# Optimization experiments

Hardware: AMD Instinct MI355X
Metric: run time of the kernel (lower is better)

## Reference

```python
import jax, jax.numpy as jnp
import numpy as np

H = 1024      # hidden_dim
NH = 8        # num_heads
DH = H // NH  # head dim = 128
IN = 512      # in_state_dim
CD = 256      # cond_dim
OUT = 512     # out_motion_dim
FH = 128      # FiLM hidden (hard-coded in _CondFiLM)
CLIP = 16.0   # input_clip
B, T = 2048, 32


def _ln(x, g, b, eps=1e-5):
    m = jnp.mean(x, axis=-1, keepdims=True)
    v = jnp.var(x, axis=-1, keepdims=True)
    return (x - m) * jax.lax.rsqrt(v + eps) * g + b


def setup_inputs() -> dict:
    key = jax.random.key(0)
    ks = jax.random.split(key, 16)
    w = lambda k, s: jax.random.normal(k, s, dtype=jnp.float32) * 0.02
    D = IN + CD
    return {
        'state': jax.random.normal(ks[0], (B, T, IN), dtype=jnp.float32),
        'cond': jax.random.normal(ks[1], (B, T, CD), dtype=jnp.float32),
        # shared_encoder: [Linear -> LayerNorm -> ReLU] x 2
        'ew1': w(ks[2], (D, H)), 'eb1': jnp.zeros((H,)), 'eg1': jnp.ones((H,)), 'ebt1': jnp.zeros((H,)),
        'ew2': w(ks[3], (H, H)), 'eb2': jnp.zeros((H,)), 'eg2': jnp.ones((H,)), 'ebt2': jnp.zeros((H,)),
        # residual_proj (input_dim != hidden_dim -> Linear)
        'rw': w(ks[4], (D, H)), 'rb': jnp.zeros((H,)),
        # FiLM conditioner
        'fw1': w(ks[5], (CD, FH)), 'fb1': jnp.zeros((FH,)),
        'fw2': w(ks[6], (FH, 2 * H)), 'fb2': jnp.zeros((2 * H,)),
        # query LayerNorm
        'lnq_g': jnp.ones((H,)), 'lnq_b': jnp.zeros((H,)),
        # attention projections (bias=False)
        'wq': w(ks[7], (H, H)), 'wk': w(ks[8], (H, H)), 'wv': w(ks[9], (H, H)), 'wo': w(ks[10], (H, H)),
        # coupling norm
        'cn_g': jnp.ones((H,)), 'cn_b': jnp.zeros((H,)),
        # motion head: Linear -> ReLU -> Linear
        'hw1': w(ks[11], (H, H)), 'hb1': jnp.zeros((H,)),
        'hw2': w(ks[12], (H, OUT)), 'hb2': jnp.zeros((OUT,)),
    }


def reference(state, cond, ew1, eb1, eg1, ebt1, ew2, eb2, eg2, ebt2, rw, rb,
              fw1, fb1, fw2, fb2, lnq_g, lnq_b, wq, wk, wv, wo, cn_g, cn_b,
              hw1, hb1, hw2, hb2):
    # input concat + guard clamp
    x = jnp.clip(jnp.concatenate([state, cond], axis=-1), -CLIP, CLIP)  # [B,T,D]
    # shared encoder
    h = jax.nn.relu(_ln(x @ ew1 + eb1, eg1, ebt1))
    h = jax.nn.relu(_ln(h @ ew2 + eb2, eg2, ebt2))                       # [B,T,H]
    res = x @ rw + rb                                                    # [B,T,H]
    # FiLM gain/bias from cond (exact-erf gelu to match torch F.gelu)
    fh = jax.nn.gelu(cond @ fw1 + fb1, approximate=False)
    g, b = jnp.split(fh @ fw2 + fb2, 2, axis=-1)
    g = 1.0 + 0.5 * jnp.tanh(g)
    b = 0.5 * jnp.tanh(b)
    # FiLM-gated query path
    qin = _ln(h, lnq_g, lnq_b) * g + b
    Bq, Tq, _ = h.shape
    q = (qin @ wq).reshape(Bq, Tq, NH, DH)
    k = (h @ wk).reshape(Bq, Tq, NH, DH)
    v = (h @ wv).reshape(Bq, Tq, NH, DH)
    scores = jnp.einsum('bqhd,bkhd->bhqk', q, k) / np.float32(np.sqrt(DH))
    attn = jax.nn.softmax(scores, axis=-1)
    o = jnp.einsum('bhqk,bkhd->bqhd', attn, v).reshape(Bq, Tq, H) @ wo
    # residual couple + norm
    h2 = _ln(h + o + res, cn_g, cn_b)
    # motion head
    m = jax.nn.relu(h2 @ hw1 + hb1)
    return m @ hw2 + hb2  # [B,T,out_motion_dim]
```

## Files before the change

### kernel.cpp

```cpp
#include <hip/hip_runtime.h>
#include <hip/hip_bf16.h>

typedef unsigned short u16;
typedef short bf16x8 __attribute__((ext_vector_type(8)));
typedef u16 u16x8 __attribute__((ext_vector_type(8)));
typedef float f32x4 __attribute__((ext_vector_type(4)));
typedef float f32x16 __attribute__((ext_vector_type(16)));

#define DEV __device__ __forceinline__

DEV u16 f2bf(float f) {
  union { float f; unsigned u; } a; a.f = f;
  unsigned r = a.u + 0x7FFFu + ((a.u >> 16) & 1u);
  return (u16)(r >> 16);
}
DEV float bf2f(u16 u) {
  union { unsigned u; float f; } a; a.u = ((unsigned)u) << 16; return a.f;
}
DEV float ftanh(float v) {
  float e = __expf(2.f * v);
  return 1.f - 2.f / (e + 1.f);
}
DEV void async16(const void* g, void* l) {
  __builtin_amdgcn_global_load_lds(
      (const __attribute__((address_space(1))) unsigned int*)g,
      (__attribute__((address_space(3))) unsigned int*)l, 16, 0, 0);
}

#define SBAR() asm volatile("s_barrier" ::: "memory")
#define WAITV(n) asm volatile("s_waitcnt vmcnt(" #n ")" ::: "memory")

__global__ __launch_bounds__(256) void transpose_cvt(const float* __restrict__ in,
                                                     u16* __restrict__ out, int K, int N) {
  __shared__ float tile[32][33];
  const int kt = blockIdx.y * 32, nt = blockIdx.x * 32;
  const int tx = threadIdx.x & 31, ty = threadIdx.x >> 5;
#pragma unroll
  for (int i = 0; i < 32; i += 8) {
    int k = kt + ty + i, n = nt + tx;
    tile[ty + i][tx] = (k < K && n < N) ? in[(long)k * N + n] : 0.f;
  }
  __syncthreads();
#pragma unroll
  for (int i = 0; i < 32; i += 8) {
    int n = nt + ty + i, k = kt + tx;
    if (n < N && k < K) out[(long)n * K + k] = f2bf(tile[tx][ty + i]);
  }
}

__global__ __launch_bounds__(256) void prep_kernel(const float* __restrict__ state,
                                                   const float* __restrict__ cond,
                                                   u16* __restrict__ xb) {
  int idx = blockIdx.x * 256 + threadIdx.x;
  int t = idx / 192, c4 = idx - t * 192;
  float4 v;
  if (c4 < 128) v = ((const float4*)state)[(long)t * 128 + c4];
  else          v = ((const float4*)cond)[(long)t * 64 + (c4 - 128)];
  ushort4 o;
  o.x = f2bf(fminf(fmaxf(v.x, -16.f), 16.f));
  o.y = f2bf(fminf(fmaxf(v.y, -16.f), 16.f));
  o.z = f2bf(fminf(fmaxf(v.z, -16.f), 16.f));
  o.w = f2bf(fminf(fmaxf(v.w, -16.f), 16.f));
  *(ushort4*)(xb + (long)t * 768 + c4 * 4) = o;
}

struct WSrc { const float* p[11]; };
__global__ __launch_bounds__(256) void init_kernel(WSrc src, u16* __restrict__ wt,
                                                   const float* __restrict__ state,
                                                   const float* __restrict__ cond,
                                                   u16* __restrict__ xb) {
  __shared__ float tile[32][33];
  const int b = blockIdx.x;
  if (b >= 8480) {
    int idx = (b - 8480) * 256 + threadIdx.x;
    int t = idx / 192, c4 = idx - t * 192;
    float4 v;
    if (c4 < 128) v = ((const float4*)state)[(long)t * 128 + c4];
    else          v = ((const float4*)cond)[(long)t * 64 + (c4 - 128)];
    ushort4 o;
    o.x = f2bf(fminf(fmaxf(v.x, -16.f), 16.f));
    o.y = f2bf(fminf(fmaxf(v.y, -16.f), 16.f));
    o.z = f2bf(fminf(fmaxf(v.z, -16.f), 16.f));
    o.w = f2bf(fminf(fmaxf(v.w, -16.f), 16.f));
    *(ushort4*)(xb + (long)t * 768 + c4 * 4) = o;
    return;
  }
  int job, base, K, N, X;
  long off;
  if      (b < 768)  { job = 0;  base = 0;    K = 768;  N = 1024; X = 32; off = 0; }
  else if (b < 1536) { job = 1;  base = 768;  K = 768;  N = 1024; X = 32; off = 786432; }
  else if (b < 2560) { job = 2;  base = 1536; K = 1024; N = 1024; X = 32; off = 1572864; }
  else if (b < 2592) { job = 3;  base = 2560; K = 256;  N = 128;  X = 4;  off = 2621440; }
  else if (b < 2848) { job = 4;  base = 2592; K = 128;  N = 2048; X = 64; off = 2654208; }
  else if (b < 3872) { job = 5;  base = 2848; K = 1024; N = 1024; X = 32; off = 2916352; }
  else if (b < 4896) { job = 6;  base = 3872; K = 1024; N = 1024; X = 32; off = 3964928; }
  else if (b < 5920) { job = 7;  base = 4896; K = 1024; N = 1024; X = 32; off = 5013504; }
  else if (b < 6944) { job = 8;  base = 5920; K = 1024; N = 1024; X = 32; off = 6062080; }
  else if (b < 7968) { job = 9;  base = 6944; K = 1024; N = 1024; X = 32; off = 7110656; }
  else               { job = 10; base = 7968; K = 1024; N = 512;  X = 16; off = 8159232; }
  const float* in = src.p[job];
  u16* out = wt + off;
  const int lb = b - base;
  const int kt = (lb / X) * 32, nt = (lb % X) * 32;
  const int tx = threadIdx.x & 31, ty = threadIdx.x >> 5;
#pragma unroll
  for (int i = 0; i < 32; i += 8) {
    int k = kt + ty + i, n = nt + tx;
    tile[ty + i][tx] = (k < K && n < N) ? in[(long)k * N + n] : 0.f;
  }
  __syncthreads();
#pragma unroll
  for (int i = 0; i < 32; i += 8) {
    int n = nt + ty + i, k = kt + tx;
    if (n < N && k < K) out[(long)n * K + k] = f2bf(tile[tx][ty + i]);
  }
}

DEV void wreduce2(float& s, float& q) {
#pragma unroll
  for (int off = 32; off; off >>= 1) { s += __shfl_xor(s, off); q += __shfl_xor(q, off); }
}

__global__ __launch_bounds__(256) void ln_relu_w(const u16* in,
                                                 const float* __restrict__ g,
                                                 const float* __restrict__ bt,
                                                 u16* out) {
  const int wid = threadIdx.x >> 6, lane = threadIdx.x & 63;
  const long row = (long)blockIdx.x * 4 + wid;
  const u16* ip = in + row * 1024 + lane * 16;
  u16x8 v0 = *(const u16x8*)ip;
  u16x8 v1 = *(const u16x8*)(ip + 8);
  float x[16];
#pragma unroll
  for (int j = 0; j < 8; ++j) { x[j] = bf2f(v0[j]); x[8 + j] = bf2f(v1[j]); }
  float s = 0.f, q = 0.f;
#pragma unroll
  for (int j = 0; j < 16; ++j) { s += x[j]; q += x[j] * x[j]; }
  wreduce2(s, q);
  float mean = s * (1.f / 1024.f);
  float var  = q * (1.f / 1024.f) - mean * mean;
  float rs   = rsqrtf(var + 1e-5f);
  const int c0 = lane * 16;
  float4 g0 = *(const float4*)(g + c0),      g1 = *(const float4*)(g + c0 + 4);
  float4 g2 = *(const float4*)(g + c0 + 8),  g3 = *(const float4*)(g + c0 + 12);
  float4 b0 = *(const float4*)(bt + c0),     b1 = *(const float4*)(bt + c0 + 4);
  float4 b2 = *(const float4*)(bt + c0 + 8), b3 = *(const float4*)(bt + c0 + 12);
  float ga[16] = {g0.x,g0.y,g0.z,g0.w, g1.x,g1.y,g1.z,g1.w, g2.x,g2.y,g2.z,g2.w, g3.x,g3.y,g3.z,g3.w};
  float ba[16] = {b0.x,b0.y,b0.z,b0.w, b1.x,b1.y,b1.z,b1.w, b2.x,b2.y,b2.z,b2.w, b3.x,b3.y,b3.z,b3.w};
  u16x8 o0, o1;
#pragma unroll
  for (int j = 0; j < 8; ++j) {
    o0[j] = f2bf(fmaxf((x[j] - mean) * rs * ga[j] + ba[j], 0.f));
    o1[j] = f2bf(fmaxf((x[8 + j] - mean) * rs * ga[8 + j] + ba[8 + j], 0.f));
  }
  u16* op = out + row * 1024 + lane * 16;
  *(u16x8*)op = o0;
  *(u16x8*)(op + 8) = o1;
}

__global__ __launch_bounds__(256) void h2_w(const u16* __restrict__ h,
                                            const u16* o2,
                                            const float* __restrict__ g,
                                            const float* __restrict__ bt,
                                            u16* out) {
  const int wid = threadIdx.x >> 6, lane = threadIdx.x & 63;
  const long row = (long)blockIdx.x * 4 + wid;
  const u16* hp = h + row * 1024 + lane * 16;
  const u16* op2 = o2 + row * 1024 + lane * 16;
  u16x8 a0 = *(const u16x8*)hp,  a1 = *(const u16x8*)(hp + 8);
  u16x8 c0v = *(const u16x8*)op2, c1v = *(const u16x8*)(op2 + 8);
  float x[16];
#pragma unroll
  for (int j = 0; j < 8; ++j) {
    x[j]     = bf2f(a0[j]) + bf2f(c0v[j]);
    x[8 + j] = bf2f(a1[j]) + bf2f(c1v[j]);
  }
  float s = 0.f, q = 0.f;
#pragma unroll
  for (int j = 0; j < 16; ++j) { s += x[j]; q += x[j] * x[j]; }
  wreduce2(s, q);
  float mean = s * (1.f / 1024.f);
  float var  = q * (1.f / 1024.f) - mean * mean;
  float rs   = rsqrtf(var + 1e-5f);
  const int cc = lane * 16;
  u16x8 o0, o1;
#pragma unroll
  for (int j = 0; j < 8; ++j) {
    o0[j] = f2bf((x[j] - mean) * rs * g[cc + j] + bt[cc + j]);
    o1[j] = f2bf((x[8 + j] - mean) * rs * g[cc + 8 + j] + bt[cc + 8 + j]);
  }
  u16* op = out + row * 1024 + lane * 16;
  *(u16x8*)op = o0;
  *(u16x8*)(op + 8) = o1;
}

__global__ __launch_bounds__(256) void qin_sep_kernel(const u16* __restrict__ h,
                                                      const u16* gain, const u16* bias,
                                                      const float* __restrict__ lg,
                                                      const float* __restrict__ lbt,
                                                      u16* qout) {
  __shared__ float sh[8];
  const long row = blockIdx.x;
  const int tid = threadIdx.x;
  ushort4 hv = *(const ushort4*)(h + row * 1024 + tid * 4);
  float x[4] = {bf2f(hv.x), bf2f(hv.y), bf2f(hv.z), bf2f(hv.w)};
  float s = x[0] + x[1] + x[2] + x[3];
  float q = x[0]*x[0] + x[1]*x[1] + x[2]*x[2] + x[3]*x[3];
#pragma unroll
  for (int off = 32; off; off >>= 1) { s += __shfl_xor(s, off); q += __shfl_xor(q, off); }
  const int w = tid >> 6;
  if ((tid & 63) == 0) { sh[w] = s; sh[4 + w] = q; }
  __syncthreads();
  s = sh[0] + sh[1] + sh[2] + sh[3];
  q = sh[4] + sh[5] + sh[6] + sh[7];
  float mean = s * (1.f / 1024.f);
  float var  = q * (1.f / 1024.f) - mean * mean;
  float rs   = rsqrtf(var + 1e-5f);
  ushort4 gv = *(const ushort4*)(gain + row * 1024 + tid * 4);
  ushort4 bv = *(const ushort4*)(bias + row * 1024 + tid * 4);
  const u16* gp = (const u16*)&gv;
  const u16* bp = (const u16*)&bv;
  ushort4 ov; u16* op = (u16*)&ov;
#pragma unroll
  for (int j = 0; j < 4; ++j) {
    int c = tid * 4 + j;
    float y = (x[j] - mean) * rs * lg[c] + lbt[c];
    op[j] = f2bf(y * bf2f(gp[j]) + bf2f(bp[j]));
  }
  *(ushort4*)(qout + row * 1024 + tid * 4) = ov;
}

__global__ __launch_bounds__(256) void film_qin(const u16* __restrict__ hbf,
                                                const u16* __restrict__ fh,
                                                const u16* __restrict__ fw2T,
                                                const float* __restrict__ fb2,
                                                const float* __restrict__ lg,
                                                const float* __restrict__ lbt,
                                                u16* __restrict__ qout) {
  extern __shared__ char lds[];
  u16* H = (u16*)lds;
  char* Afh = lds + 65536;
  float* sLN = (float*)(lds + 73728);
  const int tid = threadIdx.x;
  const int wid = tid >> 6, lane = tid & 63;
  const int fr = lane & 15, fq = lane >> 4;
  const long rows0 = (long)blockIdx.x * 32;

  {
    const int row = tid >> 3;
    const int inner = (tid & 7) * 32;
    const u16* src = fh + (rows0 + row) * 128 + (tid & 7) * 16;
    u16x8 f0 = *(const u16x8*)src;
    u16x8 f1 = *(const u16x8*)(src + 8);
    *(u16x8*)(Afh + row * 256 + ((inner)      ^ ((row & 7) << 4))) = f0;
    *(u16x8*)(Afh + row * 256 + ((inner + 16) ^ ((row & 7) << 4))) = f1;
  }

#pragma unroll
  for (int i = 0; i < 8; ++i) {
    const int row = i * 4 + wid;
    const u16* src = hbf + (rows0 + row) * 1024 + lane * 16;
    u16x8 v0 = *(const u16x8*)src;
    u16x8 v1 = *(const u16x8*)(src + 8);
    *(u16x8*)(H + row * 1024 + lane * 16) = v0;
    *(u16x8*)(H + row * 1024 + lane * 16 + 8) = v1;
    float s = 0.f, q = 0.f;
#pragma unroll
    for (int j = 0; j < 8; ++j) {
      float x0 = bf2f(v0[j]), x1 = bf2f(v1[j]);
      s += x0 + x1; q += x0 * x0 + x1 * x1;
    }
    wreduce2(s, q);
    if (lane == 0) {
      float mean = s * (1.f / 1024.f);
      float var  = q * (1.f / 1024.f) - mean * mean;
      sLN[row * 2] = mean;
      sLN[row * 2 + 1] = rsqrtf(var + 1e-5f);
    }
  }
  __syncthreads();

  const int cbase = wid * 256;
#pragma unroll 1
  for (int c8 = 0; c8 < 16; ++c8) {
    const int c = cbase + c8 * 16;
    const int col = c + fr;
    f32x4 ag[2] = {{0.f,0.f,0.f,0.f},{0.f,0.f,0.f,0.f}};
    f32x4 ab[2] = {{0.f,0.f,0.f,0.f},{0.f,0.f,0.f,0.f}};
#pragma unroll
    for (int ks = 0; ks < 4; ++ks) {
      bf16x8 bg = *(const bf16x8*)(fw2T + (long)col * 128 + ks * 32 + fq * 8);
      bf16x8 bb = *(const bf16x8*)(fw2T + (long)(1024 + col) * 128 + ks * 32 + fq * 8);
#pragma unroll
      for (int t = 0; t < 2; ++t) {
        const int row = t * 16 + fr;
        bf16x8 av = *(const bf16x8*)(Afh + row * 256 + ((ks * 64 + fq * 16) ^ ((fr & 7) << 4)));
        ag[t] = __builtin_amdgcn_mfma_f32_16x16x32_bf16(av, bg, ag[t], 0, 0, 0);
        ab[t] = __builtin_amdgcn_mfma_f32_16x16x32_bf16(av, bb, ab[t], 0, 0, 0);
      }
    }
    const float fg = fb2[col], fb = fb2[1024 + col];
    const float lgc = lg[col], lbc = lbt[col];
#pragma unroll
    for (int t = 0; t < 2; ++t)
#pragma unroll
      for (int r = 0; r < 4; ++r) {
        const int row = t * 16 + fq * 4 + r;
        float gv = 1.f + 0.5f * ftanh(ag[t][r] + fg);
        float bv = 0.5f * ftanh(ab[t][r] + fb);
        float x = bf2f(H[row * 1024 + col]);
        float y = (x - sLN[row * 2]) * sLN[row * 2 + 1] * lgc + lbc;
        H[row * 1024 + col] = f2bf(y * gv + bv);
      }
  }
  __syncthreads();

#pragma unroll
  for (int i = 0; i < 8; ++i) {
    const int row = i * 4 + wid;
    u16* dst = qout + (rows0 + row) * 1024 + lane * 16;
    *(u16x8*)dst = *(const u16x8*)(H + row * 1024 + lane * 16);
    *(u16x8*)(dst + 8) = *(const u16x8*)(H + row * 1024 + lane * 16 + 8);
  }
}

template <int EPI>
__global__ __launch_bounds__(256) void gemm_bt(const u16* __restrict__ A,
                                               const u16* __restrict__ Bt,
                                               const float* __restrict__ bias,
                                               const u16* addend,
                                               u16* Co, float* Cf,
                                               int N, int K, int lda) {
  __shared__ u16 As[128 * 64];
  __shared__ u16 Bs[128 * 64];
  const int tid = threadIdx.x;
  const int w = tid >> 6, l = tid & 63;
  const int wr = w >> 1, wc = w & 1;
  const long bRow = (long)blockIdx.x * 128;
  const long bCol = (long)blockIdx.y * 128;

  f32x4 acc[4][4];
#pragma unroll
  for (int mi = 0; mi < 4; ++mi)
#pragma unroll
    for (int ni = 0; ni < 4; ++ni) acc[mi][ni] = (f32x4){0.f, 0.f, 0.f, 0.f};

  const int arow = l >> 3;
  const int acol = (l & 7) * 8;
  const u16* gA = A + (bRow + w * 8 + arow) * (long)lda + acol;
  const u16* gB = Bt + (bCol + w * 8 + arow) * (long)K + acol;

  const int fr = l & 15;
  const int fks = (l >> 4) * 8;

  for (int kt = 0; kt < K; kt += 64) {
#pragma unroll
    for (int i = 0; i < 4; ++i) {
      async16(gA + (long)i * 32 * lda + kt, As + (i * 32 + w * 8) * 64);
      async16(gB + (long)i * 32 * K   + kt, Bs + (i * 32 + w * 8) * 64);
    }
    __syncthreads();
#pragma unroll
    for (int kk = 0; kk < 2; ++kk) {
      const int ko = kk * 32 + fks;
      bf16x8 af[4], bff[4];
#pragma unroll
      for (int mi = 0; mi < 4; ++mi)
        af[mi] = *(const bf16x8*)(As + (wr * 64 + mi * 16 + fr) * 64 + ko);
#pragma unroll
      for (int ni = 0; ni < 4; ++ni)
        bff[ni] = *(const bf16x8*)(Bs + (wc * 64 + ni * 16 + fr) * 64 + ko);
#pragma unroll
      for (int mi = 0; mi < 4; ++mi)
#pragma unroll
        for (int ni = 0; ni < 4; ++ni)
          acc[mi][ni] = __builtin_amdgcn_mfma_f32_16x16x32_bf16(af[mi], bff[ni], acc[mi][ni], 0, 0, 0);
    }
    __syncthreads();
  }

  const int fq = l >> 4;
#pragma unroll
  for (int ni = 0; ni < 4; ++ni) {
    const long col = bCol + wc * 64 + ni * 16 + fr;
    const float bs = bias ? bias[col] : 0.f;
#pragma unroll
    for (int mi = 0; mi < 4; ++mi) {
#pragma unroll
      for (int r = 0; r < 4; ++r) {
        const long row = bRow + wr * 64 + mi * 16 + fq * 4 + r;
        float v = acc[mi][ni][r] + bs;
        if (EPI == 1) v = 0.5f * v * (1.f + erff(v * 0.70710678118654752f));
        else if (EPI == 2) v = 1.f + 0.5f * ftanh(v);
        else if (EPI == 3) v = fmaxf(v, 0.f);
        else if (EPI == 5) v += bf2f(addend[row * N + col]);
        else if (EPI == 6) v = 0.5f * ftanh(v);
        if (EPI == 4) Cf[row * N + col] = v;
        else          Co[row * N + col] = f2bf(v);
      }
    }
  }
}


#define RDA(buf, Qr) do { \
  _Pragma("unroll") for (int ks_ = 0; ks_ < 2; ++ks_) \
  _Pragma("unroll") for (int m_ = 0; m_ < 4; ++m_) \
    a[ks_][m_] = *(const bf16x8*)(ldsc + (buf) * 32768 + \
      ((Qr) * 128 + wr * 64 + m_ * 16 + fr) * 128 + ((ks_ * 64 + fq * 16) ^ swzc)); \
} while (0)

#define RDB(buf, Qc, bb) do { \
  _Pragma("unroll") for (int ks_ = 0; ks_ < 2; ++ks_) \
  _Pragma("unroll") for (int n_ = 0; n_ < 2; ++n_) \
    bb[ks_][n_] = *(const bf16x8*)(ldsc + 65536 + (buf) * 32768 + \
      ((Qc) * 128 + wc * 32 + n_ * 16 + fr) * 128 + ((ks_ * 64 + fq * 16) ^ swzc)); \
} while (0)

#define MM(Qr, Qc, bb) do { \
  __builtin_amdgcn_s_setprio(1); \
  _Pragma("unroll") for (int m_ = 0; m_ < 4; ++m_) \
  _Pragma("unroll") for (int n_ = 0; n_ < 2; ++n_) \
  _Pragma("unroll") for (int ks_ = 0; ks_ < 2; ++ks_) \
    acc[Qr][Qc][m_][n_] = __builtin_amdgcn_mfma_f32_16x16x32_bf16( \
        a[ks_][m_], bb[ks_][n_], acc[Qr][Qc][m_][n_], 0, 0, 0); \
  __builtin_amdgcn_s_setprio(0); \
} while (0)

#define STA(buf, tt, h) do { \
  _Pragma("unroll") for (int j_ = 0; j_ < 2; ++j_) \
    async16(aB + ((long)j_ * 64 + (h) * 128) * lda_l + (tt) * 64, \
            ldsc + (buf) * 32768 + (h) * 16384 + (j_ * 512 + tid) * 16); \
} while (0)

#define STB(buf, tt, h) do { \
  _Pragma("unroll") for (int j_ = 0; j_ < 2; ++j_) \
    async16(bB + ((long)j_ * 64 + (h) * 128) * K_l + (tt) * 64, \
            ldsc + 65536 + (buf) * 32768 + (h) * 16384 + (j_ * 512 + tid) * 16); \
} while (0)

template <int EPI>
__global__ __launch_bounds__(512, 2) void gemm256(const u16* __restrict__ A,
                                                  const u16* __restrict__ Bt,
                                                  const float* __restrict__ bias,
                                                  const u16* addend,
                                                  u16* Co, u16* Co2, float* Cf,
                                                  int N, int K, int lda, int ctLog) {
  extern __shared__ char ldsc[];
  const int tid = threadIdx.x;
  const int l = tid & 63;
  const int w = tid >> 6, wr = w >> 2, wc = w & 3;
  const int fr = l & 15, fq = l >> 4;
  const int swzc = (fr & 7) << 4;
  const long lda_l = lda, K_l = K;

  const int nwg = gridDim.x;
  const int orig = blockIdx.x;
  const int swz = (orig & 7) * (nwg >> 3) + (orig >> 3);
  const int rt = swz >> ctLog, ct = swz & ((1 << ctLog) - 1);
  const long bRow = (long)rt * 256, bCol = (long)ct * 256;
  const int NT = K >> 6;

  const int L0 = tid * 16;
  const int row0 = L0 >> 7;
  const int cswz = (L0 & 127) ^ ((row0 & 7) << 4);
  const u16* aB = A + (bRow + row0) * lda_l + (cswz >> 1);
  const u16* bB = Bt + (bCol + row0) * K_l + (cswz >> 1);

  f32x4 acc[2][2][4][2];
#pragma unroll
  for (int p = 0; p < 2; ++p)
#pragma unroll
    for (int qq = 0; qq < 2; ++qq)
#pragma unroll
      for (int m = 0; m < 4; ++m)
#pragma unroll
        for (int n = 0; n < 2; ++n) acc[p][qq][m][n] = (f32x4){0.f, 0.f, 0.f, 0.f};

  bf16x8 a[2][4], b0[2][2], b1[2][2];

  STA(0, 0, 0); STA(0, 0, 1); STB(0, 0, 0); STB(0, 0, 1);
  STA(1, 1, 0); STB(1, 1, 1);
  WAITV(4);
  SBAR();

  for (int i = 0; i < (NT >> 1); ++i) {
    const int t0 = 2 * i, t1 = t0 + 1;
    const bool more = (t0 + 2) < NT;
    RDA(0, 0); RDB(0, 0, b0); RDB(0, 1, b1);
    STA(1, t1, 1); STB(1, t1, 0);
    SBAR(); MM(0, 0, b0); MM(0, 1, b1); SBAR();
    RDA(0, 1);
    if (more) { STA(0, t0 + 2, 0); STB(0, t0 + 2, 1); }
    SBAR(); MM(1, 1, b1); MM(1, 0, b0);
    if (more) { WAITV(4); } else { WAITV(0); }
    SBAR();
    RDA(1, 0); RDB(1, 0, b0); RDB(1, 1, b1);
    if (more) { STA(0, t0 + 2, 1); STB(0, t0 + 2, 0); }
    SBAR(); MM(0, 0, b0); MM(0, 1, b1); SBAR();
    RDA(1, 1);
    if (more) { STA(1, t1 + 2, 0); STB(1, t1 + 2, 1); }
    SBAR(); MM(1, 1, b1); MM(1, 0, b0);
    if (more) { WAITV(4); } else { WAITV(0); }
    SBAR();
  }

  if (EPI != 4) {
    u16* dst = Co; long colBase = bCol; long strideW = N;
    if (EPI == 6) {
      strideW = 1024;
      if (bCol >= 1024) { dst = Co2; colBase = bCol - 1024; }
    }
    u16* lds16 = (u16*)ldsc;
#pragma unroll
    for (int Qr = 0; Qr < 2; ++Qr)
#pragma unroll
      for (int Qc = 0; Qc < 2; ++Qc)
#pragma unroll
        for (int n = 0; n < 2; ++n) {
          const int colL = Qc * 128 + wc * 32 + n * 16 + fr;
          const float bs = bias ? bias[bCol + colL] : 0.f;
#pragma unroll
          for (int m = 0; m < 4; ++m)
#pragma unroll
            for (int r = 0; r < 4; ++r) {
              const int rowL = Qr * 128 + wr * 64 + m * 16 + fq * 4 + r;
              float v = acc[Qr][Qc][m][n][r] + bs;
              if (EPI == 3) v = fmaxf(v, 0.f);
              lds16[rowL * 256 + colL] = f2bf(v);
            }
        }
    __syncthreads();
    const int rB = tid >> 5, cL = (tid & 31) * 8;
#pragma unroll
    for (int it = 0; it < 16; ++it) {
      const int rL = it * 16 + rB;
      const long gr = bRow + rL;
      u16x8 sv = *(const u16x8*)(lds16 + rL * 256 + cL);
      if (EPI == 5) {
        u16x8 ad = *(const u16x8*)(addend + gr * (long)N + bCol + cL);
#pragma unroll
        for (int j = 0; j < 8; ++j) sv[j] = f2bf(bf2f(sv[j]) + bf2f(ad[j]));
      }
      *(u16x8*)(dst + gr * strideW + colBase + cL) = sv;
    }
  } else {
    float* ldsf = (float*)ldsc;
#pragma unroll
    for (int p = 0; p < 2; ++p) {
#pragma unroll
      for (int Qc = 0; Qc < 2; ++Qc)
#pragma unroll
        for (int n = 0; n < 2; ++n) {
          const int colL = Qc * 128 + wc * 32 + n * 16 + fr;
          const float bs = bias ? bias[bCol + colL] : 0.f;
#pragma unroll
          for (int m = 0; m < 4; ++m)
#pragma unroll
            for (int r = 0; r < 4; ++r) {
              const int rowL = wr * 64 + m * 16 + fq * 4 + r;
              ldsf[rowL * 256 + colL] = acc[p][Qc][m][n][r] + bs;
            }
        }
      __syncthreads();
      const int c4 = (tid & 63) * 4, rB = tid >> 6;
#pragma unroll
      for (int it = 0; it < 16; ++it) {
        const int rL = it * 8 + rB;
        const long gr = bRow + p * 128 + rL;
        float4 fv = *(const float4*)(ldsf + rL * 256 + c4);
        *(float4*)(Cf + gr * (long)N + bCol + c4) = fv;
      }
      __syncthreads();
    }
  }
}

__global__ __launch_bounds__(256) void attn4_kernel(const u16* q,
                                                    const u16* __restrict__ k,
                                                    const u16* __restrict__ v,
                                                    u16* o) {
  const int tid = threadIdx.x;
  const int wid = tid >> 6, l = tid & 63;
  const int bh = blockIdx.x * 4 + wid;
  const int b = bh >> 3, hd = bh & 7;
  const long base = (long)b * 32 * 1024 + hd * 128;
  const int lo = l & 31, hi = l >> 5;
  __shared__ u16 P[4][32 * 36];
  __shared__ u16 Vt[4][128 * 36];
  u16* Pw = P[wid];
  u16* Vw = Vt[wid];

#pragma unroll
  for (int i = 0; i < 8; ++i) {
    int idx = i * 64 + l;
    int tok = idx >> 4, d0 = (idx & 15) * 8;
    const u16* src = v + base + (long)tok * 1024 + d0;
    ushort4 a0 = *(const ushort4*)src;
    ushort4 a1 = *(const ushort4*)(src + 4);
    u16 vals[8] = {a0.x, a0.y, a0.z, a0.w, a1.x, a1.y, a1.z, a1.w};
#pragma unroll
    for (int j = 0; j < 8; ++j) Vw[(d0 + j) * 36 + tok] = vals[j];
  }

  f32x16 st;
#pragma unroll
  for (int r = 0; r < 16; ++r) st[r] = 0.f;
#pragma unroll
  for (int kb = 0; kb < 8; ++kb) {
    bf16x8 kf = *(const bf16x8*)(k + base + (long)lo * 1024 + kb * 16 + hi * 8);
    bf16x8 qf = *(const bf16x8*)(q + base + (long)lo * 1024 + kb * 16 + hi * 8);
    st = __builtin_amdgcn_mfma_f32_32x32x16_bf16(kf, qf, st, 0, 0, 0);
  }
  float mx = -1e30f;
#pragma unroll
  for (int r = 0; r < 16; ++r) { st[r] *= 0.08838834764831845f; mx = fmaxf(mx, st[r]); }
  mx = fmaxf(mx, __shfl_xor(mx, 32));
  float p[16], sum = 0.f;
#pragma unroll
  for (int r = 0; r < 16; ++r) { p[r] = __expf(st[r] - mx); sum += p[r]; }
  sum += __shfl_xor(sum, 32);
  const float inv = 1.f / sum;
#pragma unroll
  for (int r = 0; r < 16; ++r) {
    int kt = (r & 3) + 8 * (r >> 2) + 4 * hi;
    Pw[lo * 36 + kt] = f2bf(p[r] * inv);
  }
  __syncthreads();

#pragma unroll
  for (int nb = 0; nb < 4; ++nb) {
    f32x16 oa;
#pragma unroll
    for (int r = 0; r < 16; ++r) oa[r] = 0.f;
#pragma unroll
    for (int ks = 0; ks < 2; ++ks) {
      union { bf16x8 v8; ushort4 h[2]; } pa, vb;
      pa.h[0] = *(const ushort4*)&Pw[lo * 36 + ks * 16 + hi * 8];
      pa.h[1] = *(const ushort4*)&Pw[lo * 36 + ks * 16 + hi * 8 + 4];
      vb.h[0] = *(const ushort4*)&Vw[(nb * 32 + lo) * 36 + ks * 16 + hi * 8];
      vb.h[1] = *(const ushort4*)&Vw[(nb * 32 + lo) * 36 + ks * 16 + hi * 8 + 4];
      oa = __builtin_amdgcn_mfma_f32_32x32x16_bf16(pa.v8, vb.v8, oa, 0, 0, 0);
    }
#pragma unroll
    for (int r = 0; r < 16; ++r) {
      int qrow = (r & 3) + 8 * (r >> 2) + 4 * hi;
      o[base + (long)qrow * 1024 + nb * 32 + lo] = f2bf(oa[r]);
    }
  }
}

extern "C" void kernel_launch(void* const* d_in, const int* in_sizes, int n_in,
                              void* d_out, int out_size, void* d_ws, size_t ws_size,
                              hipStream_t stream) {
  const float* state = (const float*)d_in[0];  const float* cond  = (const float*)d_in[1];
  const float* ew1 = (const float*)d_in[2];    const float* eb1 = (const float*)d_in[3];
  const float* eg1 = (const float*)d_in[4];    const float* ebt1 = (const float*)d_in[5];
  const float* ew2 = (const float*)d_in[6];    const float* eb2 = (const float*)d_in[7];
  const float* eg2 = (const float*)d_in[8];    const float* ebt2 = (const float*)d_in[9];
  const float* rw = (const float*)d_in[10];    const float* rb = (const float*)d_in[11];
  const float* fw1 = (const float*)d_in[12];   const float* fb1 = (const float*)d_in[13];
  const float* fw2 = (const float*)d_in[14];   const float* fb2 = (const float*)d_in[15];
  const float* lnq_g = (const float*)d_in[16]; const float* lnq_b = (const float*)d_in[17];
  const float* wq = (const float*)d_in[18];    const float* wk = (const float*)d_in[19];
  const float* wv = (const float*)d_in[20];    const float* wo = (const float*)d_in[21];
  const float* cn_g = (const float*)d_in[22];  const float* cn_b = (const float*)d_in[23];
  const float* hw1 = (const float*)d_in[24];   const float* hb1 = (const float*)d_in[25];
  const float* hw2 = (const float*)d_in[26];   const float* hb2 = (const float*)d_in[27];

  const size_t MB128 = 134217728ULL;
  const size_t WT_BYTES = 17367040ULL;
  const size_t FH_BYTES = 16777216ULL;
  char* ws = (char*)d_ws;
  u16* OUTu = (u16*)d_out;
  float* OUTf = (float*)d_out;

  (void)hipFuncSetAttribute((const void*)gemm256<0>, hipFuncAttributeMaxDynamicSharedMemorySize, 131072);
  (void)hipFuncSetAttribute((const void*)gemm256<3>, hipFuncAttributeMaxDynamicSharedMemorySize, 131072);
  (void)hipFuncSetAttribute((const void*)gemm256<4>, hipFuncAttributeMaxDynamicSharedMemorySize, 131072);
  (void)hipFuncSetAttribute((const void*)gemm256<5>, hipFuncAttributeMaxDynamicSharedMemorySize, 131072);
  (void)hipFuncSetAttribute((const void*)gemm256<6>, hipFuncAttributeMaxDynamicSharedMemorySize, 131072);
  (void)hipFuncSetAttribute((const void*)film_qin,   hipFuncAttributeMaxDynamicSharedMemorySize, 73984);

  u16* wt = nullptr;
  bool planA = false;
  int R = 0;
  if (ws_size >= 3 * MB128 + FH_BYTES + WT_BYTES) {
    planA = true;
    wt = (u16*)(ws + 3 * MB128 + FH_BYTES);
  } else {
    for (int r = 8192; r >= 1024; r >>= 1) {
      size_t need = 2 * MB128 + (size_t)r * 8448ULL + WT_BYTES;
      if (ws_size >= need) { R = r; wt = (u16*)(ws + 2 * MB128 + (size_t)r * 8448ULL); break; }
    }
    if (!R) return;
  }

  u16* ew1T = wt + 0;        u16* rwT  = wt + 786432;  u16* ew2T = wt + 1572864;
  u16* fw1T = wt + 2621440;  u16* fw2T = wt + 2654208;
  u16* wqT  = wt + 2916352;  u16* wkT  = wt + 3964928; u16* wvT  = wt + 5013504;
  u16* woT  = wt + 6062080;  u16* hw1T = wt + 7110656; u16* hw2T = wt + 8159232;

  if (planA) {
    u16* S1 = (u16*)ws;
    u16* S2 = (u16*)(ws + MB128);
    u16* S3 = (u16*)(ws + 2 * MB128);
    u16* FH = (u16*)(ws + 3 * MB128);

    WSrc src;
    src.p[0] = ew1; src.p[1] = rw;  src.p[2] = ew2; src.p[3] = fw1; src.p[4] = fw2;
    src.p[5] = wq;  src.p[6] = wk;  src.p[7] = wv;  src.p[8] = wo;  src.p[9] = hw1;
    src.p[10] = hw2;
    init_kernel<<<57632, 256, 0, stream>>>(src, wt, state, cond, S1);

    gemm_bt<1><<<dim3(512, 1), 256, 0, stream>>>(S1 + 512, fw1T, fb1, nullptr, FH, nullptr, 128, 256, 768);
    gemm256<0><<<1024, 512, 131072, stream>>>(S1, ew1T, eb1, nullptr, S2, nullptr, nullptr, 1024, 768, 768, 2);
    ln_relu_w<<<16384, 256, 0, stream>>>(S2, eg1, ebt1, S2);
    gemm256<0><<<1024, 512, 131072, stream>>>(S2, ew2T, eb2, nullptr, S3, nullptr, nullptr, 1024, 1024, 1024, 2);
    ln_relu_w<<<16384, 256, 0, stream>>>(S3, eg2, ebt2, S3);
    film_qin<<<2048, 256, 73984, stream>>>(S3, FH, fw2T, fb2, lnq_g, lnq_b, OUTu);
    gemm256<0><<<1024, 512, 131072, stream>>>(OUTu, wqT, nullptr, nullptr, S1, nullptr, nullptr, 1024, 1024, 1024, 2);
    gemm256<6><<<2048, 512, 131072, stream>>>(S3, wkT, nullptr, nullptr, S2, OUTu, nullptr, 2048, 1024, 1024, 3);
    attn4_kernel<<<4096, 256, 0, stream>>>(S1, S2, OUTu, S1);
    prep_kernel<<<49152, 256, 0, stream>>>(state, cond, S2);
    gemm256<0><<<1024, 512, 131072, stream>>>(S2, rwT, rb, nullptr, OUTu, nullptr, nullptr, 1024, 768, 768, 2);
    gemm256<5><<<1024, 512, 131072, stream>>>(S1, woT, nullptr, OUTu, OUTu, nullptr, nullptr, 1024, 1024, 1024, 2);
    h2_w<<<16384, 256, 0, stream>>>(S3, OUTu, cn_g, cn_b, S1);
    gemm256<3><<<1024, 512, 131072, stream>>>(S1, hw1T, hb1, nullptr, S2, nullptr, nullptr, 1024, 1024, 1024, 2);
    gemm256<4><<<512, 512, 131072, stream>>>(S2, hw2T, hb2, nullptr, nullptr, nullptr, OUTf, 512, 1024, 1024, 1);
    return;
  }

  transpose_cvt<<<dim3(32, 24), 256, 0, stream>>>(ew1, ew1T, 768, 1024);
  transpose_cvt<<<dim3(32, 24), 256, 0, stream>>>(rw,  rwT,  768, 1024);
  transpose_cvt<<<dim3(32, 32), 256, 0, stream>>>(ew2, ew2T, 1024, 1024);
  transpose_cvt<<<dim3(4, 8),   256, 0, stream>>>(fw1, fw1T, 256, 128);
  transpose_cvt<<<dim3(64, 4),  256, 0, stream>>>(fw2, fw2T, 128, 2048);
  transpose_cvt<<<dim3(32, 32), 256, 0, stream>>>(wq, wqT, 1024, 1024);
  transpose_cvt<<<dim3(32, 32), 256, 0, stream>>>(wk, wkT, 1024, 1024);
  transpose_cvt<<<dim3(32, 32), 256, 0, stream>>>(wv, wvT, 1024, 1024);
  transpose_cvt<<<dim3(32, 32), 256, 0, stream>>>(wo, woT, 1024, 1024);
  transpose_cvt<<<dim3(32, 32), 256, 0, stream>>>(hw1, hw1T, 1024, 1024);
  transpose_cvt<<<dim3(16, 32), 256, 0, stream>>>(hw2, hw2T, 1024, 512);

  u16* F1 = (u16*)ws;
  u16* F2 = (u16*)(ws + MB128);
  char* g = ws + 2 * MB128;
  u16* G0 = (u16*)g;
  u16* G1 = (u16*)(g + (size_t)R * 2048);
  u16* G2 = (u16*)(g + (size_t)R * 4096);
  u16* G3 = (u16*)(g + (size_t)R * 4096 + (size_t)R * 256);
  u16* G4 = (u16*)(g + (size_t)R * 6144 + (size_t)R * 256);
  const int GX = R / 128, CH = 65536 / R;

  for (int c = 0; c < CH; ++c) {
    const long r0 = (long)c * R;
    prep_kernel<<<R * 3 / 4, 256, 0, stream>>>(state + r0 * 512, cond + r0 * 256, G0);
    gemm_bt<1><<<dim3(GX, 1), 256, 0, stream>>>(G0 + 512, fw1T, fb1, nullptr, G2, nullptr, 128, 256, 768);
    gemm_bt<0><<<dim3(GX, 8), 256, 0, stream>>>(G0, ew1T, eb1, nullptr, G1, nullptr, 1024, 768, 768);
    gemm_bt<0><<<dim3(GX, 8), 256, 0, stream>>>(G0, rwT,  rb,  nullptr, F2 + r0 * 1024, nullptr, 1024, 768, 768);
    ln_relu_w<<<R / 4, 256, 0, stream>>>(G1, eg1, ebt1, G3);
    gemm_bt<0><<<dim3(GX, 8), 256, 0, stream>>>(G3, ew2T, eb2, nullptr, G0, nullptr, 1024, 1024, 1024);
    ln_relu_w<<<R / 4, 256, 0, stream>>>(G0, eg2, ebt2, F1 + r0 * 1024);
    gemm_bt<2><<<dim3(GX, 8), 256, 0, stream>>>(G2, fw2T, fb2, nullptr, G3, nullptr, 1024, 128, 128);
    gemm_bt<6><<<dim3(GX, 8), 256, 0, stream>>>(G2, fw2T + 131072, fb2 + 1024, nullptr, G1, nullptr, 1024, 128, 128);
    qin_sep_kernel<<<R, 256, 0, stream>>>(F1 + r0 * 1024, G3, G1, lnq_g, lnq_b, G3);
    gemm_bt<0><<<dim3(GX, 8), 256, 0, stream>>>(G3, wqT, nullptr, nullptr, G0, nullptr, 1024, 1024, 1024);
    gemm_bt<0><<<dim3(GX, 8), 256, 0, stream>>>(F1 + r0 * 1024, wkT, nullptr, nullptr, G1, nullptr, 1024, 1024, 1024);
    gemm_bt<0><<<dim3(GX, 8), 256, 0, stream>>>(F1 + r0 * 1024, wvT, nullptr, nullptr, G4, nullptr, 1024, 1024, 1024);
    attn4_kernel<<<R / 16, 256, 0, stream>>>(G0, G1, G4, G0);
    gemm_bt<5><<<dim3(GX, 8), 256, 0, stream>>>(G0, woT, nullptr, F2 + r0 * 1024, F2 + r0 * 1024, nullptr, 1024, 1024, 1024);
  }
  h2_w<<<16384, 256, 0, stream>>>(F1, F2, cn_g, cn_b, OUTu);
  gemm_bt<3><<<dim3(512, 8), 256, 0, stream>>>(OUTu, hw1T, hb1, nullptr, F1, nullptr, 1024, 1024, 1024);
  gemm_bt<4><<<dim3(512, 4), 256, 0, stream>>>(F1, hw2T, hb2, nullptr, nullptr, OUTf, 512, 1024, 1024);
}
```

Measured before the change: 1.943 ms.

## Double-buffer LDS fragment registers to overlap reads with MFMA in gemm256

Restructures the main loop of the 256x256 GEMM so that A/B fragments are read from LDS into a second register set while MFMAs run on the first set (ping-pong aP/aS, bP/bS). The global-to-LDS async loads are regrouped by half-tile, with waits and barriers interleaved between quadrant MFMA blocks. The aim is to hide LDS read latency and barrier stalls behind matrix math. It costs more VGPRs, which may hurt occupancy under the 512x2 launch bounds, and the reordered waits and barriers add a risk of LDS races.

```diff
diff --git a/kernel.cpp b/kernel.cpp
--- a/kernel.cpp
+++ b/kernel.cpp
@@ -403,27 +403,27 @@
 }
 
 
-#define RDA(buf, Qr) do { \
+#define RDA(buf, Qr, dst) do { \
   _Pragma("unroll") for (int ks_ = 0; ks_ < 2; ++ks_) \
   _Pragma("unroll") for (int m_ = 0; m_ < 4; ++m_) \
-    a[ks_][m_] = *(const bf16x8*)(ldsc + (buf) * 32768 + \
+    dst[ks_][m_] = *(const bf16x8*)(ldsc + (buf) * 32768 + \
       ((Qr) * 128 + wr * 64 + m_ * 16 + fr) * 128 + ((ks_ * 64 + fq * 16) ^ swzc)); \
 } while (0)
 
-#define RDB(buf, Qc, bb) do { \
+#define RDB(buf, Qc, dst) do { \
   _Pragma("unroll") for (int ks_ = 0; ks_ < 2; ++ks_) \
   _Pragma("unroll") for (int n_ = 0; n_ < 2; ++n_) \
-    bb[ks_][n_] = *(const bf16x8*)(ldsc + 65536 + (buf) * 32768 + \
+    dst[ks_][n_] = *(const bf16x8*)(ldsc + 65536 + (buf) * 32768 + \
       ((Qc) * 128 + wc * 32 + n_ * 16 + fr) * 128 + ((ks_ * 64 + fq * 16) ^ swzc)); \
 } while (0)
 
-#define MM(Qr, Qc, bb) do { \
+#define MM(Qr, Qc, aa, bb) do { \
   __builtin_amdgcn_s_setprio(1); \
   _Pragma("unroll") for (int m_ = 0; m_ < 4; ++m_) \
   _Pragma("unroll") for (int n_ = 0; n_ < 2; ++n_) \
   _Pragma("unroll") for (int ks_ = 0; ks_ < 2; ++ks_) \
     acc[Qr][Qc][m_][n_] = __builtin_amdgcn_mfma_f32_16x16x32_bf16( \
-        a[ks_][m_], bb[ks_][n_], acc[Qr][Qc][m_][n_], 0, 0, 0); \
+        aa[ks_][m_], bb[ks_][n_], acc[Qr][Qc][m_][n_], 0, 0, 0); \
   __builtin_amdgcn_s_setprio(0); \
 } while (0)
 
@@ -477,31 +477,45 @@
 #pragma unroll
         for (int n = 0; n < 2; ++n) acc[p][qq][m][n] = (f32x4){0.f, 0.f, 0.f, 0.f};
 
-  bf16x8 a[2][4], b0[2][2], b1[2][2];
+  bf16x8 aP[2][4], aS[2][4], bP[2][2], bS[2][2];
 
   STA(0, 0, 0); STA(0, 0, 1); STB(0, 0, 0); STB(0, 0, 1);
-  STA(1, 1, 0); STB(1, 1, 1);
-  WAITV(4);
+  STA(1, 1, 0); STA(1, 1, 1); STB(1, 1, 0); STB(1, 1, 1);
+  WAITV(8);
   SBAR();
+  RDA(0, 0, aP); RDB(0, 0, bP);
 
   for (int i = 0; i < (NT >> 1); ++i) {
-    const int t0 = 2 * i, t1 = t0 + 1;
-    const bool more = (t0 + 2) < NT;
-    RDA(0, 0); RDB(0, 0, b0); RDB(0, 1, b1);
-    STA(1, t1, 1); STB(1, t1, 0);
-    SBAR(); MM(0, 0, b0); MM(0, 1, b1); SBAR();
-    RDA(0, 1);
-    if (more) { STA(0, t0 + 2, 0); STB(0, t0 + 2, 1); }
-    SBAR(); MM(1, 1, b1); MM(1, 0, b0);
-    if (more) { WAITV(4); } else { WAITV(0); }
+    const int t2 = 2 * i + 2, t3 = t2 + 1;
+    const bool more = t2 < NT;
+    RDB(0, 1, bS);
+    MM(0, 0, aP, bP);
     SBAR();
-    RDA(1, 0); RDB(1, 0, b0); RDB(1, 1, b1);
-    if (more) { STA(0, t0 + 2, 1); STB(0, t0 + 2, 0); }
-    SBAR(); MM(0, 0, b0); MM(0, 1, b1); SBAR();
-    RDA(1, 1);
-    if (more) { STA(1, t1 + 2, 0); STB(1, t1 + 2, 1); }
-    SBAR(); MM(1, 1, b1); MM(1, 0, b0);
-    if (more) { WAITV(4); } else { WAITV(0); }
+    RDA(0, 1, aS);
+    MM(0, 1, aP, bS);
+    SBAR();
+    if (more) { STA(0, t2, 0); STB(0, t2, 0); WAITV(4); }
+    else      { WAITV(0); }
+    MM(1, 1, aS, bS);
+    SBAR();
+    RDA(1, 0, aP); RDB(1, 0, bS);
+    if (more) { STA(0, t2, 1); STB(0, t2, 1); }
+    MM(1, 0, aS, bP);
+    SBAR();
+    RDB(1, 1, bP);
+    MM(0, 0, aP, bS);
+    SBAR();
+    RDA(1, 1, aS);
+    MM(0, 1, aP, bP);
+    SBAR();
+    if (more) { STA(1, t3, 0); STB(1, t3, 0); WAITV(4); }
+    MM(1, 1, aS, bP);
+    SBAR();
+    if (more) {
+      RDA(0, 0, aP); RDB(0, 0, bP);
+      STA(1, t3, 1); STB(1, t3, 1);
+    }
+    MM(1, 0, aS, bS);
     SBAR();
   }
 
```

New measurement: 3.172 ms. 63.3% more time.
